# Kernel tuning notes

Measured on AMD Instinct MI355X. Metric: run time of the kernel, lower is better.

The kernel has to match this reference:

```python
import jax, jax.numpy as jnp
import numpy as np

WS = 8  # window size
NH = 4  # heads
EPS = 1e-5

def _rel_pos_index(ws):
    coords = np.stack(np.meshgrid(np.arange(ws), np.arange(ws), indexing='ij')).reshape(2, -1)
    rel = coords[:, :, None] - coords[:, None, :]
    rel[0] += ws - 1
    rel[1] += ws - 1
    rel[0] *= 2 * ws - 1
    return jnp.asarray(rel.sum(0))  # (ws*ws, ws*ws) int

REL_IDX = _rel_pos_index(WS)

def group_norm1(x, g, b):
    # GroupNorm(1, C): normalize over (C,H,W) per sample, per-channel affine
    m = jnp.mean(x, axis=(1, 2, 3), keepdims=True)
    v = jnp.var(x, axis=(1, 2, 3), keepdims=True)
    return (x - m) * jax.lax.rsqrt(v + EPS) * g[None, :, None, None] + b[None, :, None, None]

def conv1x1(x, w, b):
    return jnp.einsum('oc,bchw->bohw', w, x) + b[None, :, None, None]

def win_attn(x, qkv_w, qkv_b, out_w, out_b, bias_tab):
    # x: (B,H,W,C); non-shifted Swin window attention with gathered rel-pos bias
    B, H, W, C = x.shape
    hd = C // NH
    L = WS * WS
    scale = hd ** -0.5
    nh_, nw_ = H // WS, W // WS
    xw = x.reshape(B, nh_, WS, nw_, WS, C).transpose(0, 1, 3, 2, 4, 5).reshape(-1, L, C)
    qkv = (xw @ qkv_w.T + qkv_b).reshape(-1, L, 3, NH, hd)
    q = jnp.transpose(qkv[:, :, 0], (0, 2, 1, 3))  # (N,NH,L,hd)
    k = jnp.transpose(qkv[:, :, 1], (0, 2, 1, 3))
    v = jnp.transpose(qkv[:, :, 2], (0, 2, 1, 3))
    bias = bias_tab[:, REL_IDX.reshape(-1)].reshape(NH, L, L)
    attn = jax.nn.softmax(jnp.einsum('nhqd,nhkd->nhqk', q, k) * scale + bias[None], axis=-1)
    o = jnp.einsum('nhqk,nhkd->nhqd', attn, v).transpose(0, 2, 1, 3).reshape(-1, L, C)
    o = o @ out_w.T + out_b
    return o.reshape(B, nh_, nw_, WS, WS, C).transpose(0, 1, 3, 2, 4, 5).reshape(B, H, W, C)

def ffn(x, g, b, w1, b1, w2, b2):
    h = group_norm1(x, g, b)
    h = jax.nn.gelu(conv1x1(h, w1, b1), approximate=False)
    return conv1x1(h, w2, b2)

def setup_inputs() -> dict:
    key = jax.random.key(0)
    B, D, H, W = 8, 192, 128, 128
    ks = jax.random.split(key, 16)
    s = 0.02
    return {
        'sem': jax.random.normal(ks[0], (B, D, H, W), jnp.float32),
        'depth_feat': jax.random.normal(ks[1], (B, D, H, W), jnp.float32),
        'ns_g': jnp.ones((D,), jnp.float32), 'ns_b': jnp.zeros((D,), jnp.float32),
        'nd_g': jnp.ones((D,), jnp.float32), 'nd_b': jnp.zeros((D,), jnp.float32),
        'wd2s': jax.random.normal(ks[2], (D, D), jnp.float32) * s, 'bd2s': jnp.zeros((D,), jnp.float32),
        'ws2d': jax.random.normal(ks[3], (D, D), jnp.float32) * s, 'bs2d': jnp.zeros((D,), jnp.float32),
        'alpha': jnp.float32(0.1), 'beta': jnp.float32(0.1),
        'qkv_sem_w': jax.random.normal(ks[4], (3 * D, D), jnp.float32) * s, 'qkv_sem_b': jnp.zeros((3 * D,), jnp.float32),
        'out_sem_w': jax.random.normal(ks[5], (D, D), jnp.float32) * s, 'out_sem_b': jnp.zeros((D,), jnp.float32),
        'qkv_dep_w': jax.random.normal(ks[6], (3 * D, D), jnp.float32) * s, 'qkv_dep_b': jnp.zeros((3 * D,), jnp.float32),
        'out_dep_w': jax.random.normal(ks[7], (D, D), jnp.float32) * s, 'out_dep_b': jnp.zeros((D,), jnp.float32),
        'rel_pos_bias': jax.random.normal(ks[8], (NH, (2 * WS - 1) ** 2), jnp.float32) * s,
        'fs_g': jnp.ones((D,), jnp.float32), 'fs_b': jnp.zeros((D,), jnp.float32),
        'fs_w1': jax.random.normal(ks[9], (2 * D, D), jnp.float32) * s, 'fs_b1': jnp.zeros((2 * D,), jnp.float32),
        'fs_w2': jax.random.normal(ks[10], (D, 2 * D), jnp.float32) * s, 'fs_b2': jnp.zeros((D,), jnp.float32),
        'fd_g': jnp.ones((D,), jnp.float32), 'fd_b': jnp.zeros((D,), jnp.float32),
        'fd_w1': jax.random.normal(ks[11], (2 * D, D), jnp.float32) * s, 'fd_b1': jnp.zeros((2 * D,), jnp.float32),
        'fd_w2': jax.random.normal(ks[12], (D, 2 * D), jnp.float32) * s, 'fd_b2': jnp.zeros((D,), jnp.float32),
    }

def reference(sem, depth_feat, ns_g, ns_b, nd_g, nd_b, wd2s, bd2s, ws2d, bs2d, alpha, beta,
              qkv_sem_w, qkv_sem_b, out_sem_w, out_sem_b, qkv_dep_w, qkv_dep_b, out_dep_w, out_dep_b,
              rel_pos_bias, fs_g, fs_b, fs_w1, fs_b1, fs_w2, fs_b2, fd_g, fd_b, fd_w1, fd_b1, fd_w2, fd_b2):
    sem_n = group_norm1(sem, ns_g, ns_b)
    depth_n = group_norm1(depth_feat, nd_g, nd_b)
    sem_in = sem_n + alpha * jax.nn.sigmoid(conv1x1(depth_n, wd2s, bd2s))
    dep_in = depth_n + beta * jax.nn.sigmoid(conv1x1(sem_n, ws2d, bs2d))
    sem_hw = jnp.transpose(sem_in, (0, 2, 3, 1))  # (B,H,W,C)
    dep_hw = jnp.transpose(dep_in, (0, 2, 3, 1))
    sem_a = win_attn(sem_hw, qkv_sem_w, qkv_sem_b, out_sem_w, out_sem_b, rel_pos_bias)
    dep_a = win_attn(dep_hw, qkv_dep_w, qkv_dep_b, out_dep_w, out_dep_b, rel_pos_bias)
    sem_out = sem + jnp.transpose(sem_a, (0, 3, 1, 2))
    dep_out = depth_feat + jnp.transpose(dep_a, (0, 3, 1, 2))
    sem_out = sem_out + ffn(sem_out, fs_g, fs_b, fs_w1, fs_b1, fs_w2, fs_b2)
    dep_out = dep_out + ffn(dep_out, fd_g, fd_b, fd_w1, fd_b1, fd_w2, fd_b2)
    return (sem_out, dep_out)
```

## Files before the change

### kernel.cpp

```cpp
#include <hip/hip_runtime.h>

typedef unsigned short u16;
typedef float f32x4 __attribute__((ext_vector_type(4)));
typedef int   i32x4 __attribute__((ext_vector_type(4)));
typedef short bf16x8 __attribute__((ext_vector_type(8)));

#define CCH    192
#define HW     16384
#define NPIX   131072
#define NELEM  25165824
#define NSAMP  3145728

__device__ __forceinline__ float b2f(u16 u) {
  return __uint_as_float(((unsigned)u) << 16);
}
__device__ __forceinline__ u16 f2b(float f) {
  unsigned u = __float_as_uint(f);
  unsigned r = (u + 0x7fffu + ((u >> 16) & 1u)) >> 16;
  return (u16)r;
}
__device__ __forceinline__ void unpack8(i32x4 v, float* f) {
#pragma unroll
  for (int i = 0; i < 4; i++) {
    unsigned u = (unsigned)v[i];
    f[2 * i]     = __uint_as_float(u << 16);
    f[2 * i + 1] = __uint_as_float(u & 0xffff0000u);
  }
}
__device__ __forceinline__ i32x4 pack8(const float* f) {
  i32x4 r;
#pragma unroll
  for (int i = 0; i < 4; i++) {
    unsigned lo = f2b(f[2 * i]);
    unsigned hi = f2b(f[2 * i + 1]);
    r[i] = (int)(lo | (hi << 16));
  }
  return r;
}

__global__ __launch_bounds__(256) void stats_partial(
    const float* __restrict__ A, const float* __restrict__ B,
    float* __restrict__ acc, int slotbase) {
  const float* src = (blockIdx.z == 0) ? A : B;
  int sample = blockIdx.y;
  size_t base = (size_t)sample * NSAMP + (size_t)blockIdx.x * 32768;
  float s = 0.f, q = 0.f;
  for (int it = 0; it < 16; it++) {
    const float* ptr = src + base + it * 2048 + threadIdx.x * 8;
    f32x4 v0 = *(const f32x4*)ptr;
    f32x4 v1 = *(const f32x4*)(ptr + 4);
#pragma unroll
    for (int i = 0; i < 4; i++) {
      s += v0[i] + v1[i];
      q += v0[i] * v0[i] + v1[i] * v1[i];
    }
  }
#pragma unroll
  for (int o = 32; o > 0; o >>= 1) {
    s += __shfl_down(s, o);
    q += __shfl_down(q, o);
  }
  __shared__ float red[8];
  int wv = threadIdx.x >> 6;
  if ((threadIdx.x & 63) == 0) { red[wv * 2] = s; red[wv * 2 + 1] = q; }
  __syncthreads();
  if (threadIdx.x == 0) {
    float S = red[0] + red[2] + red[4] + red[6];
    float Q = red[1] + red[3] + red[5] + red[7];
    int e = ((slotbase + blockIdx.z) * 8 + sample) * 2;
    atomicAdd(&acc[e], S);
    atomicAdd(&acc[e + 1], Q);
  }
}

__global__ void finalize_stats(const float* __restrict__ acc,
                               float* __restrict__ mr, int entbase, int nent) {
  int i = threadIdx.x;
  if (i < nent) {
    int e = entbase + i;
    float s = acc[e * 2], q = acc[e * 2 + 1];
    const float invN = 1.0f / (float)NSAMP;
    float mean = s * invN;
    float var = q * invN - mean * mean;
    mr[e * 2] = mean;
    mr[e * 2 + 1] = rsqrtf(var + 1e-5f);
  }
}

__global__ __launch_bounds__(256) void norm_t(
    const float* __restrict__ in, u16* __restrict__ outp,
    const float* __restrict__ g, const float* __restrict__ bb,
    const float* __restrict__ mr, int slot) {
  __shared__ u16 tile[128 * 201];
  int yy = blockIdx.x, b = blockIdx.y;
  int e = (slot * 8 + b) * 2;
  float mean = mr[e], rstd = mr[e + 1];
  int tid = threadIdx.x;
  for (int task = tid; task < 3072; task += 256) {
    int c = task >> 4, xc = task & 15;
    const float* p = in + (size_t)(b * CCH + c) * HW + yy * 128 + xc * 8;
    f32x4 v0 = *(const f32x4*)p;
    f32x4 v1 = *(const f32x4*)(p + 4);
    float sc = rstd * g[c];
    float of = bb[c] - mean * sc;
#pragma unroll
    for (int i = 0; i < 4; i++) {
      tile[(xc * 8 + i) * 201 + c]       = f2b(v0[i] * sc + of);
      tile[(xc * 8 + 4 + i) * 201 + c]   = f2b(v1[i] * sc + of);
    }
  }
  __syncthreads();
  size_t ob = ((size_t)b * HW + (size_t)yy * 128) * CCH;
  for (int task = tid; task < 3072; task += 256) {
    int xx = task / 24, cc = task % 24;
    i32x4 v;
#pragma unroll
    for (int i = 0; i < 4; i++) {
      unsigned lo = tile[xx * 201 + cc * 8 + 2 * i];
      unsigned hi = tile[xx * 201 + cc * 8 + 2 * i + 1];
      v[i] = (int)(lo | (hi << 16));
    }
    *(i32x4*)(outp + ob + (size_t)xx * CCH + cc * 8) = v;
  }
}

__global__ __launch_bounds__(256) void attn_kernel(
    const u16* __restrict__ qkv, const float* __restrict__ relb,
    u16* __restrict__ outp) {
  __shared__ u16 kbuf[64 * 200];
  __shared__ u16 vbuf[64 * 200];
  __shared__ float btab[900];
  int tid = threadIdx.x;
  int h = tid >> 6, t = tid & 63;
  int win = blockIdx.x;
  int b = win >> 8, wy = (win >> 4) & 15, wx = win & 15;
  int ty = t >> 3, tx = t & 7;
  int y = wy * 8 + ty, x = wx * 8 + tx;
  int p = (b << 14) + y * 128 + x;
  for (int i = tid; i < 900; i += 256) btab[i] = relb[i];
  const u16* qp = qkv + (size_t)p * 576 + h * 48;
  float qreg[48];
#pragma unroll
  for (int c = 0; c < 6; c++) {
    i32x4 v = *(const i32x4*)(qp + c * 8);
    unpack8(v, &qreg[c * 8]);
  }
  const float scale = 0.14433756729740643f;
#pragma unroll
  for (int i = 0; i < 48; i++) qreg[i] *= scale;
  int rb = t * 200 + h * 48;
#pragma unroll
  for (int c = 0; c < 6; c++) {
    *(i32x4*)&kbuf[rb + c * 8] = *(const i32x4*)(qp + 192 + c * 8);
    *(i32x4*)&vbuf[rb + c * 8] = *(const i32x4*)(qp + 384 + c * 8);
  }
  __syncthreads();
  float oacc[48];
#pragma unroll
  for (int i = 0; i < 48; i++) oacc[i] = 0.f;
  float l = 0.f;
  int hb = h * 225 + (ty + 7) * 15 + tx + 7;
  for (int j = 0; j < 64; j++) {
    const u16* kr = &kbuf[j * 200 + h * 48];
    float s0 = 0.f, s1 = 0.f, s2 = 0.f, s3 = 0.f;
#pragma unroll
    for (int c = 0; c < 6; c++) {
      i32x4 kv = *(const i32x4*)(kr + c * 8);
      float kf[8];
      unpack8(kv, kf);
      s0 += qreg[c * 8 + 0] * kf[0]; s1 += qreg[c * 8 + 1] * kf[1];
      s2 += qreg[c * 8 + 2] * kf[2]; s3 += qreg[c * 8 + 3] * kf[3];
      s0 += qreg[c * 8 + 4] * kf[4]; s1 += qreg[c * 8 + 5] * kf[5];
      s2 += qreg[c * 8 + 6] * kf[6]; s3 += qreg[c * 8 + 7] * kf[7];
    }
    int jy = j >> 3, jx = j & 7;
    float sv = (s0 + s1) + (s2 + s3) + btab[hb - jy * 15 - jx];
    sv = fminf(fmaxf(sv, -60.f), 60.f);
    float e = __expf(sv);
    l += e;
    const u16* vr = &vbuf[j * 200 + h * 48];
#pragma unroll
    for (int c = 0; c < 6; c++) {
      i32x4 vv = *(const i32x4*)(vr + c * 8);
      float vf[8];
      unpack8(vv, vf);
#pragma unroll
      for (int i2 = 0; i2 < 8; i2++) oacc[c * 8 + i2] += e * vf[i2];
    }
  }
  float rl = 1.0f / l;
  u16* op = outp + (size_t)p * CCH + h * 48;
#pragma unroll
  for (int c = 0; c < 6; c++) {
    float f[8];
#pragma unroll
    for (int i2 = 0; i2 < 8; i2++) f[i2] = oacc[c * 8 + i2] * rl;
    *(i32x4*)(op + c * 8) = pack8(f);
  }
}

enum { GM_BIAS = 0, GM_GATE = 1, GM_GELU = 2, GM_RES = 3 };

struct SmemGemm {
  union {
    struct { u16 xs[64 * 72]; u16 ws[64 * 72]; } s;
    float y[64 * 72];
  };
};

template <int MODE>
__global__ __launch_bounds__(256) void gemm_kernel(
    const u16* __restrict__ X, const float* __restrict__ W,
    const float* __restrict__ bias, const void* aux,
    void* outv, const float* __restrict__ scale_ptr, int K, int O) {
  __shared__ SmemGemm sm;
  int tid = threadIdx.x;
  int p0 = blockIdx.x * 64;
  int o0 = blockIdx.y * 64;
  int lane = tid & 63, wave = tid >> 6;
  int l15 = lane & 15, q8 = lane >> 4;
  int wm = (wave & 1) * 32, wn = (wave >> 1) * 32;

  f32x4 acc[2][2];
#pragma unroll
  for (int i = 0; i < 2; i++)
#pragma unroll
    for (int j = 0; j < 2; j++) {
      f32x4 z = {0.f, 0.f, 0.f, 0.f};
      acc[i][j] = z;
    }

  int srow = tid >> 2;
  int scol = (tid & 3) * 16;
  const u16* xg   = X + (size_t)(p0 + srow) * K + scol;
  const float* wg = W + (size_t)(o0 + srow) * K + scol;
  u16* xst = &sm.s.xs[srow * 72 + scol];
  u16* wst = &sm.s.ws[srow * 72 + scol];

  for (int k0 = 0; k0 < K; k0 += 64) {
    __syncthreads();
    i32x4 x0 = *(const i32x4*)xg;
    i32x4 x1 = *(const i32x4*)(xg + 8);
    f32x4 wv0 = *(const f32x4*)wg;
    f32x4 wv1 = *(const f32x4*)(wg + 4);
    f32x4 wv2 = *(const f32x4*)(wg + 8);
    f32x4 wv3 = *(const f32x4*)(wg + 12);
    xg += 64; wg += 64;
    float wf[16];
#pragma unroll
    for (int i = 0; i < 4; i++) {
      wf[i] = wv0[i]; wf[4 + i] = wv1[i]; wf[8 + i] = wv2[i]; wf[12 + i] = wv3[i];
    }
    *(i32x4*)xst = x0;
    *(i32x4*)(xst + 8) = x1;
    *(i32x4*)wst = pack8(wf);
    *(i32x4*)(wst + 8) = pack8(wf + 8);
    __syncthreads();
#pragma unroll
    for (int s = 0; s < 2; s++) {
      bf16x8 a0 = *(const bf16x8*)&sm.s.xs[(wm + l15) * 72 + s * 32 + q8 * 8];
      bf16x8 a1 = *(const bf16x8*)&sm.s.xs[(wm + 16 + l15) * 72 + s * 32 + q8 * 8];
      bf16x8 b0 = *(const bf16x8*)&sm.s.ws[(wn + l15) * 72 + s * 32 + q8 * 8];
      bf16x8 b1 = *(const bf16x8*)&sm.s.ws[(wn + 16 + l15) * 72 + s * 32 + q8 * 8];
      acc[0][0] = __builtin_amdgcn_mfma_f32_16x16x32_bf16(a0, b0, acc[0][0], 0, 0, 0);
      acc[0][1] = __builtin_amdgcn_mfma_f32_16x16x32_bf16(a0, b1, acc[0][1], 0, 0, 0);
      acc[1][0] = __builtin_amdgcn_mfma_f32_16x16x32_bf16(a1, b0, acc[1][0], 0, 0, 0);
      acc[1][1] = __builtin_amdgcn_mfma_f32_16x16x32_bf16(a1, b1, acc[1][1], 0, 0, 0);
    }
  }
  __syncthreads();
#pragma unroll
  for (int mi = 0; mi < 2; mi++) {
#pragma unroll
    for (int ni = 0; ni < 2; ni++) {
      int pl = wm + mi * 16 + q8 * 4;
      int ol = wn + ni * 16 + l15;
#pragma unroll
      for (int r = 0; r < 4; r++) {
        float v = acc[mi][ni][r];
        if (MODE == GM_RES) sm.y[ol * 72 + pl + r] = v;
        else                sm.y[(pl + r) * 72 + ol] = v;
      }
    }
  }
  __syncthreads();
  if (MODE == GM_RES) {
    const float* auxf = (const float*)aux;
    float* outf = (float*)outv;
    int o = tid >> 2;
    int pc = (tid & 3) * 16;
    float vals[16];
#pragma unroll
    for (int i = 0; i < 16; i++) vals[i] = sm.y[o * 72 + pc + i];
    int og = o0 + o;
    int pg = p0 + pc;
    int bi = pg >> 14;
    int r = pg & (HW - 1);
    size_t idx = ((size_t)(bi * CCH + og) << 14) + r;
    float bv = bias[og];
    f32x4 res[4];
#pragma unroll
    for (int i = 0; i < 4; i++) res[i] = *(const f32x4*)(auxf + idx + i * 4);
#pragma unroll
    for (int i = 0; i < 4; i++) {
      f32x4 w;
#pragma unroll
      for (int j = 0; j < 4; j++) w[j] = res[i][j] + vals[i * 4 + j] + bv;
      *(f32x4*)(outf + idx + i * 4) = w;
    }
  } else {
    u16* outb = (u16*)outv;
    const u16* auxb = (const u16*)aux;
    int pl = tid >> 2;
    int oc = (tid & 3) * 16;
    float vals[16];
#pragma unroll
    for (int i = 0; i < 16; i++) vals[i] = sm.y[pl * 72 + oc + i];
    int og0 = o0 + oc;
    size_t rowb = (size_t)(p0 + pl) * (size_t)O + og0;
    float sc = 0.f;
    if (MODE == GM_GATE) sc = scale_ptr[0];
    float f[16];
#pragma unroll
    for (int i = 0; i < 16; i++) {
      float v = vals[i] + bias[og0 + i];
      if (MODE == GM_GATE) {
        float sg = 1.0f / (1.0f + __expf(-v));
        v = b2f(auxb[rowb + i]) + sc * sg;
      } else if (MODE == GM_GELU) {
        v = 0.5f * v * (1.0f + erff(v * 0.70710678118654752f));
      }
      f[i] = v;
    }
    *(i32x4*)(outb + rowb) = pack8(f);
    *(i32x4*)(outb + rowb + 8) = pack8(f + 8);
  }
}

extern "C" void kernel_launch(void* const* d_in, const int* in_sizes, int n_in,
                              void* d_out, int out_size, void* d_ws,
                              size_t ws_size, hipStream_t stream) {
  (void)in_sizes; (void)n_in; (void)out_size; (void)ws_size;
  const float* sem       = (const float*)d_in[0];
  const float* dep       = (const float*)d_in[1];
  const float* ns_g      = (const float*)d_in[2];
  const float* ns_b      = (const float*)d_in[3];
  const float* nd_g      = (const float*)d_in[4];
  const float* nd_b      = (const float*)d_in[5];
  const float* wd2s      = (const float*)d_in[6];
  const float* bd2s      = (const float*)d_in[7];
  const float* ws2d      = (const float*)d_in[8];
  const float* bs2d      = (const float*)d_in[9];
  const float* alpha     = (const float*)d_in[10];
  const float* beta      = (const float*)d_in[11];
  const float* qkv_sem_w = (const float*)d_in[12];
  const float* qkv_sem_b = (const float*)d_in[13];
  const float* out_sem_w = (const float*)d_in[14];
  const float* out_sem_b = (const float*)d_in[15];
  const float* qkv_dep_w = (const float*)d_in[16];
  const float* qkv_dep_b = (const float*)d_in[17];
  const float* out_dep_w = (const float*)d_in[18];
  const float* out_dep_b = (const float*)d_in[19];
  const float* relb      = (const float*)d_in[20];
  const float* fs_g      = (const float*)d_in[21];
  const float* fs_b      = (const float*)d_in[22];
  const float* fs_w1     = (const float*)d_in[23];
  const float* fs_b1     = (const float*)d_in[24];
  const float* fs_w2     = (const float*)d_in[25];
  const float* fs_b2     = (const float*)d_in[26];
  const float* fd_g      = (const float*)d_in[27];
  const float* fd_b      = (const float*)d_in[28];
  const float* fd_w1     = (const float*)d_in[29];
  const float* fd_b1     = (const float*)d_in[30];
  const float* fd_w2     = (const float*)d_in[31];
  const float* fd_b2     = (const float*)d_in[32];

  float* stats_acc = (float*)d_ws;
  float* mr        = (float*)((char*)d_ws + 256);
  u16* R1 = (u16*)((char*)d_ws + 1024);
  u16* R2 = R1 + NELEM;
  u16* R3 = R2 + NELEM;
  u16* R4 = R3 + NELEM;
  u16* R5 = R4 + NELEM;
  float* outS = (float*)d_out;
  float* outD = outS + NELEM;

  hipMemsetAsync(d_ws, 0, 512, stream);
  stats_partial<<<dim3(96, 8, 2), 256, 0, stream>>>(sem, dep, stats_acc, 0);
  finalize_stats<<<1, 64, 0, stream>>>(stats_acc, mr, 0, 16);
  norm_t<<<dim3(128, 8), 256, 0, stream>>>(sem, R1, ns_g, ns_b, mr, 0);
  norm_t<<<dim3(128, 8), 256, 0, stream>>>(dep, R2, nd_g, nd_b, mr, 1);
  gemm_kernel<GM_GATE><<<dim3(2048, 3), 256, 0, stream>>>(R2, wd2s, bd2s, R1, R3, alpha, 192, 192);
  gemm_kernel<GM_GATE><<<dim3(2048, 3), 256, 0, stream>>>(R1, ws2d, bs2d, R2, R4, beta, 192, 192);
  gemm_kernel<GM_BIAS><<<dim3(2048, 9), 256, 0, stream>>>(R3, qkv_sem_w, qkv_sem_b, nullptr, R5, nullptr, 192, 576);
  attn_kernel<<<2048, 256, 0, stream>>>(R5, relb, R2);
  gemm_kernel<GM_RES><<<dim3(2048, 3), 256, 0, stream>>>(R2, out_sem_w, out_sem_b, sem, outS, nullptr, 192, 192);
  gemm_kernel<GM_BIAS><<<dim3(2048, 9), 256, 0, stream>>>(R4, qkv_dep_w, qkv_dep_b, nullptr, R5, nullptr, 192, 576);
  attn_kernel<<<2048, 256, 0, stream>>>(R5, relb, R2);
  gemm_kernel<GM_RES><<<dim3(2048, 3), 256, 0, stream>>>(R2, out_dep_w, out_dep_b, dep, outD, nullptr, 192, 192);
  stats_partial<<<dim3(96, 8, 2), 256, 0, stream>>>(outS, outD, stats_acc, 2);
  finalize_stats<<<1, 64, 0, stream>>>(stats_acc, mr, 16, 16);
  norm_t<<<dim3(128, 8), 256, 0, stream>>>(outS, R1, fs_g, fs_b, mr, 2);
  norm_t<<<dim3(128, 8), 256, 0, stream>>>(outD, R3, fd_g, fd_b, mr, 3);
  gemm_kernel<GM_GELU><<<dim3(2048, 6), 256, 0, stream>>>(R1, fs_w1, fs_b1, nullptr, R5, nullptr, 192, 384);
  gemm_kernel<GM_RES><<<dim3(2048, 3), 256, 0, stream>>>(R5, fs_w2, fs_b2, outS, outS, nullptr, 384, 192);
  gemm_kernel<GM_GELU><<<dim3(2048, 6), 256, 0, stream>>>(R3, fd_w1, fd_b1, nullptr, R5, nullptr, 192, 384);
  gemm_kernel<GM_RES><<<dim3(2048, 3), 256, 0, stream>>>(R5, fd_w2, fd_b2, outD, outD, nullptr, 384, 192);
}
```

Measured before the change: 1.898 ms.

## Rewrite window attention with bf16 MFMA for QK^T and PV

Replaces the per-thread scalar FP32 attention loop with MFMA 16x16x32 bf16 matrix instructions. Each wavefront handles one head for a 64-token window, with K padded to 64 channels (zeroed) and V stored transposed in LDS. A small pre-kernel writes the relative-position bias in MFMA register layout into a workspace buffer (reusing R1). Probabilities are rounded to bf16 before the PV product, which costs some precision. Normalisation is done with cross-lane shuffles.

New measurement: 1.692 ms. -10.9%, faster.

```diff
diff --git a/kernel.cpp b/kernel.cpp
--- a/kernel.cpp
+++ b/kernel.cpp
@@ -124,78 +124,173 @@
   }
 }
 
+__global__ void build_bias(const float* __restrict__ relb,
+                           float* __restrict__ biasx) {
+  int tid = threadIdx.x;
+  for (int i = tid; i < 16384; i += 256) {
+    int r    = i & 3;
+    int lane = (i >> 2) & 63;
+    int nj   = (i >> 8) & 3;
+    int mi   = (i >> 10) & 3;
+    int h    = (i >> 12) & 3;
+    int q = 16 * mi + (lane >> 4) * 4 + r;
+    int k = 16 * nj + (lane & 15);
+    int qy = q >> 3, qx = q & 7, ky = k >> 3, kx = k & 7;
+    biasx[i] = relb[h * 225 + (qy - ky + 7) * 15 + (qx - kx + 7)];
+  }
+}
+
 __global__ __launch_bounds__(256) void attn_kernel(
-    const u16* __restrict__ qkv, const float* __restrict__ relb,
+    const u16* __restrict__ qkv, const float* __restrict__ biasx,
     u16* __restrict__ outp) {
-  __shared__ u16 kbuf[64 * 200];
-  __shared__ u16 vbuf[64 * 200];
-  __shared__ float btab[900];
+  __shared__ u16 kp[4][64 * 72];
+  __shared__ u16 vt[4][48 * 72];
   int tid = threadIdx.x;
-  int h = tid >> 6, t = tid & 63;
+  int h = tid >> 6, lane = tid & 63;
+  int l15 = lane & 15, g4 = lane >> 4;
   int win = blockIdx.x;
   int b = win >> 8, wy = (win >> 4) & 15, wx = win & 15;
-  int ty = t >> 3, tx = t & 7;
-  int y = wy * 8 + ty, x = wx * 8 + tx;
-  int p = (b << 14) + y * 128 + x;
-  for (int i = tid; i < 900; i += 256) btab[i] = relb[i];
-  const u16* qp = qkv + (size_t)p * 576 + h * 48;
-  float qreg[48];
-#pragma unroll
-  for (int c = 0; c < 6; c++) {
-    i32x4 v = *(const i32x4*)(qp + c * 8);
-    unpack8(v, &qreg[c * 8]);
-  }
+  int pbase = (b << 14) + (wy * 8) * 128 + wx * 8;
+
+  for (int task = tid; task < 1536; task += 256) {
+    int tok = task / 24;
+    int r24 = task - tok * 24;
+    int hh = r24 / 6;
+    int c = r24 - hh * 6;
+    int p = pbase + (tok >> 3) * 128 + (tok & 7);
+    i32x4 v = *(const i32x4*)(qkv + (size_t)p * 576 + 192 + hh * 48 + c * 8);
+    *(i32x4*)&kp[hh][tok * 72 + c * 8] = v;
+  }
+  {
+    i32x4 z = {0, 0, 0, 0};
+    for (int task = tid; task < 512; task += 256) {
+      int hh = task >> 7, rem = task & 127, tok = rem >> 1, c = rem & 1;
+      *(i32x4*)&kp[hh][tok * 72 + 48 + c * 8] = z;
+    }
+  }
+  for (int task = tid; task < 1536; task += 256) {
+    int chidx = task >> 6, tok = task & 63;
+    int hh = chidx / 6, c = chidx - hh * 6;
+    int p = pbase + (tok >> 3) * 128 + (tok & 7);
+    i32x4 v = *(const i32x4*)(qkv + (size_t)p * 576 + 384 + hh * 48 + c * 8);
+#pragma unroll
+    for (int i = 0; i < 4; i++) {
+      unsigned u = (unsigned)v[i];
+      vt[hh][(c * 8 + 2 * i) * 72 + tok]     = (u16)(u & 0xffffu);
+      vt[hh][(c * 8 + 2 * i + 1) * 72 + tok] = (u16)(u >> 16);
+    }
+  }
+  __syncthreads();
+
+  int ptok[4];
+#pragma unroll
+  for (int mi = 0; mi < 4; mi++) {
+    int t = 16 * mi + l15;
+    ptok[mi] = pbase + (t >> 3) * 128 + (t & 7);
+  }
+  f32x4 acc[4][4];
+#pragma unroll
+  for (int i = 0; i < 4; i++)
+#pragma unroll
+    for (int j = 0; j < 4; j++) {
+      f32x4 z = {0.f, 0.f, 0.f, 0.f};
+      acc[i][j] = z;
+    }
+#pragma unroll
+  for (int s = 0; s < 2; s++) {
+    bf16x8 qf[4], kf[4];
+#pragma unroll
+    for (int mi = 0; mi < 4; mi++)
+      qf[mi] = *(const bf16x8*)(qkv + (size_t)ptok[mi] * 576 + h * 48 + s * 32 + g4 * 8);
+#pragma unroll
+    for (int nj = 0; nj < 4; nj++)
+      kf[nj] = *(const bf16x8*)&kp[h][(16 * nj + l15) * 72 + s * 32 + g4 * 8];
+#pragma unroll
+    for (int mi = 0; mi < 4; mi++)
+#pragma unroll
+      for (int nj = 0; nj < 4; nj++)
+        acc[mi][nj] = __builtin_amdgcn_mfma_f32_16x16x32_bf16(qf[mi], kf[nj], acc[mi][nj], 0, 0, 0);
+  }
+
   const float scale = 0.14433756729740643f;
-#pragma unroll
-  for (int i = 0; i < 48; i++) qreg[i] *= scale;
-  int rb = t * 200 + h * 48;
-#pragma unroll
-  for (int c = 0; c < 6; c++) {
-    *(i32x4*)&kbuf[rb + c * 8] = *(const i32x4*)(qp + 192 + c * 8);
-    *(i32x4*)&vbuf[rb + c * 8] = *(const i32x4*)(qp + 384 + c * 8);
-  }
+  float sums[4][4];
+#pragma unroll
+  for (int mi = 0; mi < 4; mi++) {
+#pragma unroll
+    for (int r = 0; r < 4; r++) sums[mi][r] = 0.f;
+#pragma unroll
+    for (int nj = 0; nj < 4; nj++) {
+      f32x4 bv = *(const f32x4*)&biasx[(((h * 4 + mi) * 4 + nj) * 64 + lane) * 4];
+#pragma unroll
+      for (int r = 0; r < 4; r++) {
+        float sv = acc[mi][nj][r] * scale + bv[r];
+        sv = fminf(fmaxf(sv, -60.f), 60.f);
+        float e = __expf(sv);
+        acc[mi][nj][r] = e;
+        sums[mi][r] += e;
+      }
+    }
+  }
+#pragma unroll
+  for (int mi = 0; mi < 4; mi++)
+#pragma unroll
+    for (int r = 0; r < 4; r++) {
+      float s = sums[mi][r];
+      s += __shfl_xor(s, 1);
+      s += __shfl_xor(s, 2);
+      s += __shfl_xor(s, 4);
+      s += __shfl_xor(s, 8);
+      sums[mi][r] = 1.0f / s;
+    }
+#pragma unroll
+  for (int mi = 0; mi < 4; mi++)
+#pragma unroll
+    for (int nj = 0; nj < 4; nj++)
+#pragma unroll
+      for (int r = 0; r < 4; r++)
+        kp[h][(16 * mi + g4 * 4 + r) * 72 + 16 * nj + l15] = f2b(acc[mi][nj][r]);
+
+  f32x4 oacc[4][3];
+#pragma unroll
+  for (int i = 0; i < 4; i++)
+#pragma unroll
+    for (int j = 0; j < 3; j++) {
+      f32x4 z = {0.f, 0.f, 0.f, 0.f};
+      oacc[i][j] = z;
+    }
+#pragma unroll
+  for (int s = 0; s < 2; s++) {
+    bf16x8 pf[4], vf[3];
+#pragma unroll
+    for (int mi = 0; mi < 4; mi++)
+      pf[mi] = *(const bf16x8*)&kp[h][(16 * mi + l15) * 72 + s * 32 + g4 * 8];
+#pragma unroll
+    for (int n = 0; n < 3; n++)
+      vf[n] = *(const bf16x8*)&vt[h][(16 * n + l15) * 72 + s * 32 + g4 * 8];
+#pragma unroll
+    for (int mi = 0; mi < 4; mi++)
+#pragma unroll
+      for (int n = 0; n < 3; n++)
+        oacc[mi][n] = __builtin_amdgcn_mfma_f32_16x16x32_bf16(pf[mi], vf[n], oacc[mi][n], 0, 0, 0);
+  }
+
+#pragma unroll
+  for (int mi = 0; mi < 4; mi++)
+#pragma unroll
+    for (int n = 0; n < 3; n++)
+#pragma unroll
+      for (int r = 0; r < 4; r++)
+        kp[h][(16 * mi + g4 * 4 + r) * 72 + 16 * n + l15] =
+            f2b(oacc[mi][n][r] * sums[mi][r]);
   __syncthreads();
-  float oacc[48];
-#pragma unroll
-  for (int i = 0; i < 48; i++) oacc[i] = 0.f;
-  float l = 0.f;
-  int hb = h * 225 + (ty + 7) * 15 + tx + 7;
-  for (int j = 0; j < 64; j++) {
-    const u16* kr = &kbuf[j * 200 + h * 48];
-    float s0 = 0.f, s1 = 0.f, s2 = 0.f, s3 = 0.f;
-#pragma unroll
-    for (int c = 0; c < 6; c++) {
-      i32x4 kv = *(const i32x4*)(kr + c * 8);
-      float kf[8];
-      unpack8(kv, kf);
-      s0 += qreg[c * 8 + 0] * kf[0]; s1 += qreg[c * 8 + 1] * kf[1];
-      s2 += qreg[c * 8 + 2] * kf[2]; s3 += qreg[c * 8 + 3] * kf[3];
-      s0 += qreg[c * 8 + 4] * kf[4]; s1 += qreg[c * 8 + 5] * kf[5];
-      s2 += qreg[c * 8 + 6] * kf[6]; s3 += qreg[c * 8 + 7] * kf[7];
-    }
-    int jy = j >> 3, jx = j & 7;
-    float sv = (s0 + s1) + (s2 + s3) + btab[hb - jy * 15 - jx];
-    sv = fminf(fmaxf(sv, -60.f), 60.f);
-    float e = __expf(sv);
-    l += e;
-    const u16* vr = &vbuf[j * 200 + h * 48];
-#pragma unroll
-    for (int c = 0; c < 6; c++) {
-      i32x4 vv = *(const i32x4*)(vr + c * 8);
-      float vf[8];
-      unpack8(vv, vf);
-#pragma unroll
-      for (int i2 = 0; i2 < 8; i2++) oacc[c * 8 + i2] += e * vf[i2];
-    }
-  }
-  float rl = 1.0f / l;
-  u16* op = outp + (size_t)p * CCH + h * 48;
-#pragma unroll
-  for (int c = 0; c < 6; c++) {
-    float f[8];
-#pragma unroll
-    for (int i2 = 0; i2 < 8; i2++) f[i2] = oacc[c * 8 + i2] * rl;
-    *(i32x4*)(op + c * 8) = pack8(f);
+  for (int task = tid; task < 1536; task += 256) {
+    int tok = task / 24;
+    int r24 = task - tok * 24;
+    int hh = r24 / 6;
+    int c = r24 - hh * 6;
+    int p = pbase + (tok >> 3) * 128 + (tok & 7);
+    *(i32x4*)(outp + (size_t)p * 192 + hh * 48 + c * 8) =
+        *(const i32x4*)&kp[hh][tok * 72 + c * 8];
   }
 }
 
@@ -384,6 +479,7 @@
   u16* R5 = R4 + NELEM;
   float* outS = (float*)d_out;
   float* outD = outS + NELEM;
+  float* biasx = (float*)R1;
 
   hipMemsetAsync(d_ws, 0, 512, stream);
   stats_partial<<<dim3(96, 8, 2), 256, 0, stream>>>(sem, dep, stats_acc, 0);
@@ -392,11 +488,12 @@
   norm_t<<<dim3(128, 8), 256, 0, stream>>>(dep, R2, nd_g, nd_b, mr, 1);
   gemm_kernel<GM_GATE><<<dim3(2048, 3), 256, 0, stream>>>(R2, wd2s, bd2s, R1, R3, alpha, 192, 192);
   gemm_kernel<GM_GATE><<<dim3(2048, 3), 256, 0, stream>>>(R1, ws2d, bs2d, R2, R4, beta, 192, 192);
+  build_bias<<<1, 256, 0, stream>>>(relb, biasx);
   gemm_kernel<GM_BIAS><<<dim3(2048, 9), 256, 0, stream>>>(R3, qkv_sem_w, qkv_sem_b, nullptr, R5, nullptr, 192, 576);
-  attn_kernel<<<2048, 256, 0, stream>>>(R5, relb, R2);
+  attn_kernel<<<2048, 256, 0, stream>>>(R5, biasx, R2);
   gemm_kernel<GM_RES><<<dim3(2048, 3), 256, 0, stream>>>(R2, out_sem_w, out_sem_b, sem, outS, nullptr, 192, 192);
   gemm_kernel<GM_BIAS><<<dim3(2048, 9), 256, 0, stream>>>(R4, qkv_dep_w, qkv_dep_b, nullptr, R5, nullptr, 192, 576);
-  attn_kernel<<<2048, 256, 0, stream>>>(R5, relb, R2);
+  attn_kernel<<<2048, 256, 0, stream>>>(R5, biasx, R2);
   gemm_kernel<GM_RES><<<dim3(2048, 3), 256, 0, stream>>>(R2, out_dep_w, out_dep_b, dep, outD, nullptr, 192, 192);
   stats_partial<<<dim3(96, 8, 2), 256, 0, stream>>>(outS, outD, stats_acc, 2);
   finalize_stats<<<1, 64, 0, stream>>>(stats_acc, mr, 16, 16);
```
